# Kernel tuning notes

Hardware: AMD Instinct MI355X
Metric: run time of the kernel (lower is better)

Reference implementation:

```python
import jax, jax.numpy as jnp
import numpy as np
import math

H = 16          # num_heads
EPS = 1e-5      # LayerNorm eps (torch default)


def setup_inputs() -> dict:
    key = jax.random.key(0)
    ks = jax.random.split(key, 4)
    B, T, D = 2, 2048, 1024
    s = 1.0 / math.sqrt(D)
    return {
        "x": jax.random.normal(ks[0], (B, T, D), dtype=jnp.float32),
        "ln_g": jnp.ones((D,), jnp.float32),
        "ln_b": jnp.zeros((D,), jnp.float32),
        "Wq": jax.random.normal(ks[1], (D, D), jnp.float32) * s,
        "bq": jnp.zeros((D,), jnp.float32),
        "Wk": jax.random.normal(ks[2], (D, D), jnp.float32) * s,
        "bk": jnp.zeros((D,), jnp.float32),
        "Wv": jax.random.normal(ks[3], (D, D), jnp.float32) * s,
        "bv": jnp.zeros((D,), jnp.float32),
    }


def reference(x, ln_g, ln_b, Wq, bq, Wk, bk, Wv, bv):
    B, T, D = x.shape
    # LayerNorm (shared across the three projections, computed once)
    mu = jnp.mean(x, axis=-1, keepdims=True)
    var = jnp.mean(jnp.square(x - mu), axis=-1, keepdims=True)
    xn = (x - mu) * jax.lax.rsqrt(var + EPS) * ln_g + ln_b
    # Q/K/V projections -> [B, T, H, Dh]
    q = (xn @ Wq + bq).reshape(B, T, H, D // H)
    k = (xn @ Wk + bk).reshape(B, T, H, D // H)
    v = (xn @ Wv + bv).reshape(B, T, H, D // H)
    # QK^T scores [B, n, m, h], scaled by sqrt(head_dim)
    scale = 1.0 / math.sqrt(D // H)
    attn = jnp.einsum('bnhd,bmhd->bnmh', q, k) * scale
    # softmax over key axis (dim=2), dropout p=0 is identity
    w = jax.nn.softmax(attn, axis=2)
    # weighted sum of values, merge heads
    y = jnp.einsum('bnmh,bmhd->bnhd', w, v).reshape(B, T, D)
    return y
```

## Files before the change

### kernel.cpp

```cpp
#include <hip/hip_runtime.h>
#include <hip/hip_bf16.h>


typedef __attribute__((ext_vector_type(8)))  short short8;
typedef __attribute__((ext_vector_type(4)))  float f32x4;
typedef __attribute__((ext_vector_type(2)))  float f32x2;
typedef __attribute__((ext_vector_type(16))) float f32x16;
typedef __attribute__((ext_vector_type(2)))  unsigned int uint2v;

#define D_MODEL 1024
#define T_SEQ   2048
#define NHEAD   16
#define HDIM    64

#define LOG2E 1.4426950408889634f

__device__ __forceinline__ unsigned short f2bf(float x) {
    unsigned int u = __float_as_uint(x);
    u = (u + 0x7fffu + ((u >> 16) & 1u)) >> 16;
    return (unsigned short)u;
}

#if defined(__has_builtin)
#if __has_builtin(__builtin_amdgcn_permlane32_swap)
#define HAVE_PERMSWAP 1
#endif
#endif

__device__ __forceinline__ uint2v permswap(unsigned a, unsigned b) {
#ifdef HAVE_PERMSWAP
    return __builtin_amdgcn_permlane32_swap(a, b, false, false);
#else
    uint2v r;
    const unsigned as = (unsigned)__shfl_xor((int)a, 32, 64);
    const unsigned bs = (unsigned)__shfl_xor((int)b, 32, 64);
    const bool hi = (threadIdx.x & 32) != 0;
    r[0] = hi ? bs : a;
    r[1] = hi ? b  : as;
    return r;
#endif
}

__device__ __forceinline__ void group_barrier() {
    asm volatile("s_waitcnt lgkmcnt(0)" ::: "memory");
    __builtin_amdgcn_s_barrier();
    asm volatile("" ::: "memory");
}

__device__ __forceinline__ void w8(unsigned short* p, const uint4 v) {
    uint2 a; a.x = v.x; a.y = v.y;
    uint2 b; b.x = v.z; b.y = v.w;
    *(uint2*)p = a;
    *(uint2*)(p + 4) = b;
}

__device__ __forceinline__ short8 read8(const unsigned short* p) {
    union { unsigned u[4]; short8 s; } r;
    const uint2 a = *(const uint2*)p;
    const uint2 b = *(const uint2*)(p + 4);
    r.u[0] = a.x; r.u[1] = a.y; r.u[2] = b.x; r.u[3] = b.y;
    return r.s;
}

__global__ __launch_bounds__(256) void ln_wcast_kernel(
    const float* __restrict__ x, const float* __restrict__ gam,
    const float* __restrict__ bet, unsigned short* __restrict__ xn,
    const float* __restrict__ Wq, const float* __restrict__ Wk,
    const float* __restrict__ Wv, unsigned short* __restrict__ Wt)
{
    __shared__ float red[8];
    __shared__ float tile[32][33];
    const int bid = blockIdx.x;
    if (bid < 4096) {
        const int row = bid;
        const int t = threadIdx.x;
        const float4 v = ((const float4*)(x + (size_t)row * D_MODEL))[t];
        float s  = v.x + v.y + v.z + v.w;
        float s2 = v.x * v.x + v.y * v.y + v.z * v.z + v.w * v.w;
#pragma unroll
        for (int off = 32; off; off >>= 1) {
            s  += __shfl_down(s,  off, 64);
            s2 += __shfl_down(s2, off, 64);
        }
        const int lane = t & 63, wave = t >> 6;
        if (lane == 0) { red[wave] = s; red[4 + wave] = s2; }
        __syncthreads();
        s  = red[0] + red[1] + red[2] + red[3];
        s2 = red[4] + red[5] + red[6] + red[7];
        const float mu   = s * (1.f / D_MODEL);
        const float var  = s2 * (1.f / D_MODEL) - mu * mu;
        const float rstd = rsqrtf(var + 1e-5f);
        const float4 gv = ((const float4*)gam)[t];
        const float4 bv = ((const float4*)bet)[t];
        ushort4 o;
        o.x = f2bf((v.x - mu) * rstd * gv.x + bv.x);
        o.y = f2bf((v.y - mu) * rstd * gv.y + bv.y);
        o.z = f2bf((v.z - mu) * rstd * gv.z + bv.z);
        o.w = f2bf((v.w - mu) * rstd * gv.w + bv.w);
        ((ushort4*)(xn + (size_t)row * D_MODEL))[t] = o;
    } else {
        const int id = bid - 4096;
        const int z  = id >> 10;
        const int t2 = id & 1023;
        const int n0 = (t2 & 31) * 32, k0 = (t2 >> 5) * 32;
        const float* W = (z == 0) ? Wq : (z == 1) ? Wk : Wv;
        unsigned short* outw = Wt + (size_t)z * D_MODEL * D_MODEL;
        const int tx = threadIdx.x & 31, ty = threadIdx.x >> 5;
#pragma unroll
        for (int i = ty; i < 32; i += 8)
            tile[i][tx] = W[(size_t)(k0 + i) * D_MODEL + n0 + tx];
        __syncthreads();
#pragma unroll
        for (int i = ty; i < 32; i += 8)
            outw[(size_t)(n0 + i) * D_MODEL + k0 + tx] = f2bf(tile[tx][i]);
    }
}

__global__ __launch_bounds__(256) void qkv_gemm_kernel(
    const unsigned short* __restrict__ xn, const unsigned short* __restrict__ Wt,
    const float* __restrict__ bq, const float* __restrict__ bk, const float* __restrict__ bv,
    unsigned short* __restrict__ qo, unsigned short* __restrict__ ko, unsigned short* __restrict__ vt)
{
    const int which = blockIdx.x >> 3;
    const int xt = blockIdx.x & 7, yt = blockIdx.y;
    const bool vmode = (which == 2);
    const unsigned short* Aptr = vmode ? (Wt + (size_t)2 * D_MODEL * D_MODEL) : xn;
    const unsigned short* Bptr = vmode ? xn : (Wt + (size_t)which * D_MODEL * D_MODEL);
    const float* bias   = (which == 0) ? bq : (which == 1) ? bk : bv;
    const float scale   = (which == 0) ? (0.125f * LOG2E) : 1.0f;
    const int m0 = vmode ? xt * 128 : yt * 128;
    const int n0 = vmode ? yt * 128 : xt * 128;

    __shared__ unsigned short As[128][64];
    __shared__ unsigned short Bs[128][64];

    const int tid = threadIdx.x;
    const int lane = tid & 63, wave = tid >> 6;
    const int wr = wave >> 1, wc = wave & 1;
    const int g = lane >> 4, c = lane & 15;

    const int srow = lane >> 3;
    const int swzc = (((lane & 7) * 8) ^ ((srow & 7) * 8));
    const int rsw  = (c & 7) * 8;

    f32x4 acc[4][4] = {};

    for (int kt = 0; kt < D_MODEL; kt += 64) {
        __syncthreads();
#pragma unroll
        for (int i = 0; i < 4; ++i) {
            const int r = wave * 32 + i * 8;
            const unsigned short* ga = Aptr + (size_t)(m0 + r + srow) * D_MODEL + kt + swzc;
            __builtin_amdgcn_global_load_lds(
                (const __attribute__((address_space(1))) unsigned int*)ga,
                (__attribute__((address_space(3))) unsigned int*)(&As[r][0]), 16, 0, 0);
            const unsigned short* gb = Bptr + (size_t)(n0 + r + srow) * D_MODEL + kt + swzc;
            __builtin_amdgcn_global_load_lds(
                (const __attribute__((address_space(1))) unsigned int*)gb,
                (__attribute__((address_space(3))) unsigned int*)(&Bs[r][0]), 16, 0, 0);
        }
        __syncthreads();

        short8 af[4][2], bf[4][2];
#pragma unroll
        for (int i = 0; i < 4; ++i) {
            const int ra = wr * 64 + i * 16 + c;
            const int rb = wc * 64 + i * 16 + c;
#pragma unroll
            for (int kk = 0; kk < 2; ++kk) {
                af[i][kk] = *(const short8*)(&As[ra][(kk * 32 + g * 8) ^ rsw]);
                bf[i][kk] = *(const short8*)(&Bs[rb][(kk * 32 + g * 8) ^ rsw]);
            }
        }
#pragma unroll
        for (int kk = 0; kk < 2; ++kk)
#pragma unroll
            for (int i = 0; i < 4; ++i)
#pragma unroll
                for (int j = 0; j < 4; ++j)
                    acc[i][j] = __builtin_amdgcn_mfma_f32_16x16x32_bf16(
                        af[i][kk], bf[j][kk], acc[i][j], 0, 0, 0);
    }

    if (!vmode) {
        unsigned short* out = (which == 0) ? qo : ko;
#pragma unroll
        for (int j = 0; j < 4; ++j) {
            const int n = n0 + wc * 64 + j * 16 + c;
            const float bn = bias[n];
            const int h = n >> 6, dh = n & 63;
#pragma unroll
            for (int i = 0; i < 4; ++i) {
#pragma unroll
                for (int r = 0; r < 4; ++r) {
                    const int m = m0 + wr * 64 + i * 16 + g * 4 + r;
                    const int bb = m >> 11, t = m & 2047;
                    out[((size_t)(bb * NHEAD + h) * T_SEQ + t) * HDIM + dh] =
                        f2bf((acc[i][j][r] + bn) * scale);
                }
            }
        }
    } else {
#pragma unroll
        for (int i = 0; i < 4; ++i) {
#pragma unroll
            for (int r = 0; r < 4; ++r) {
                const int m = m0 + wr * 64 + i * 16 + g * 4 + r;
                const float bn = bias[m];
#pragma unroll
                for (int j = 0; j < 4; ++j) {
                    const int n = n0 + wc * 64 + j * 16 + c;
                    const int bb = n >> 11, t = n & 2047;
                    vt[(size_t)bb * (D_MODEL * T_SEQ) + (size_t)m * T_SEQ + t] =
                        f2bf(acc[i][j][r] + bn);
                }
            }
        }
    }
}

__global__ __launch_bounds__(512, 4) void attn_kernel(
    const unsigned short* __restrict__ qb, const unsigned short* __restrict__ kb,
    const unsigned short* __restrict__ vtb, float* __restrict__ out)
{
    const int id  = blockIdx.x;
    const int swz = (id & 7) * 64 + (id >> 3);
    const int qt  = swz & 15;
    const int bh  = swz >> 4;
    const int b = bh >> 4, head = bh & 15;
    const unsigned short* Q  = qb  + (size_t)bh * T_SEQ * HDIM;
    const unsigned short* Kp = kb  + (size_t)bh * T_SEQ * HDIM;
    const unsigned short* Vt = vtb + (size_t)b * (D_MODEL * T_SEQ)
                                   + (size_t)head * (HDIM * T_SEQ);

    __shared__ __align__(16) unsigned short smem[17664];

    const int tid = threadIdx.x, lane = tid & 63, wave = tid >> 6;
    const int grp = wave >> 2, w4 = wave & 3;
    const int q = lane & 31, h = lane >> 5;
    const int kvbase = grp * (T_SEQ / 2);

    const int gtid = tid & 255;
    const int sr = gtid >> 3;
    const int sc = (gtid & 7) * 8;

    unsigned short* gbase = &smem[grp * 8704];

    short8 qf[4];
    {
        const unsigned short* qp = Q + (size_t)(qt * 128 + w4 * 32 + q) * HDIM;
#pragma unroll
        for (int c = 0; c < 4; ++c)
            qf[c] = *(const short8*)(qp + c * 16 + h * 8);
    }

    float l_r = 0.f;
    f32x16 o[2] = {};

    const unsigned short* kp0 = Kp + (size_t)(kvbase + sr) * HDIM + sc;
    const unsigned short* vp0 = Vt + (size_t)sr * T_SEQ + kvbase + sc;
    uint4 kr0 = *(const uint4*)(kp0);
    uint4 kr1 = *(const uint4*)(kp0 + 32 * HDIM);
    uint4 vr0 = *(const uint4*)(vp0);
    uint4 vr1 = *(const uint4*)(vp0 + 32 * T_SEQ);
    w8(gbase + sr * 68 + sc, kr0);
    w8(gbase + (sr + 32) * 68 + sc, kr1);
    w8(gbase + 4352 + sr * 68 + sc, vr0);
    w8(gbase + 4352 + (sr + 32) * 68 + sc, vr1);
    kp0 += 64 * HDIM;
    vp0 += 64;

#pragma unroll 1
    for (int t = 0; t < 16; ++t) {
        const bool more = (t + 1 < 16);
        if (more) {
            kr0 = *(const uint4*)(kp0);
            kr1 = *(const uint4*)(kp0 + 32 * HDIM);
            vr0 = *(const uint4*)(vp0);
            vr1 = *(const uint4*)(vp0 + 32 * T_SEQ);
            kp0 += 64 * HDIM;
            vp0 += 64;
        }
        group_barrier();
        const unsigned short* kbuf = gbase;
        const unsigned short* vbuf = gbase + 4352;

        f32x16 s0 = {}, s1 = {};
        __builtin_amdgcn_s_setprio(1);
#pragma unroll
        for (int c = 0; c < 4; ++c) {
            const short8 kf0 = read8(kbuf + (size_t)q * 68 + c * 16 + h * 8);
            const short8 kf1 = read8(kbuf + (size_t)(32 + q) * 68 + c * 16 + h * 8);
            s0 = __builtin_amdgcn_mfma_f32_32x32x16_bf16(kf0, qf[c], s0, 0, 0, 0);
            s1 = __builtin_amdgcn_mfma_f32_32x32x16_bf16(kf1, qf[c], s1, 0, 0, 0);
        }
        __builtin_amdgcn_s_setprio(0);

#pragma unroll
        for (int r = 0; r < 16; ++r) { s0[r] = exp2f(s0[r]); }
#pragma unroll
        for (int r = 0; r < 16; ++r) { s1[r] = exp2f(s1[r]); }

        {
            f32x2 u[8];
#pragma unroll
            for (int r = 0; r < 8; ++r) {
                f32x2 a; a[0] = s0[2*r]; a[1] = s0[2*r+1];
                f32x2 bb; bb[0] = s1[2*r]; bb[1] = s1[2*r+1];
                u[r] = a + bb;
            }
            u[0] += u[1]; u[2] += u[3]; u[4] += u[5]; u[6] += u[7];
            u[0] += u[2]; u[4] += u[6];
            u[0] += u[4];
            float rs = u[0][0] + u[0][1];
            rs += __shfl_xor(rs, 32, 64);
            l_r += rs;
        }

        unsigned Wb0[8], Wb1[8];
#pragma unroll
        for (int u = 0; u < 4; ++u) {
            asm("v_cvt_pk_bf16_f32 %0, %1, %2" : "=v"(Wb0[u*2])   : "v"(s0[4*u]),   "v"(s0[4*u+1]));
            asm("v_cvt_pk_bf16_f32 %0, %1, %2" : "=v"(Wb0[u*2+1]) : "v"(s0[4*u+2]), "v"(s0[4*u+3]));
            asm("v_cvt_pk_bf16_f32 %0, %1, %2" : "=v"(Wb1[u*2])   : "v"(s1[4*u]),   "v"(s1[4*u+1]));
            asm("v_cvt_pk_bf16_f32 %0, %1, %2" : "=v"(Wb1[u*2+1]) : "v"(s1[4*u+2]), "v"(s1[4*u+3]));
        }

        short8 pf[4];
#pragma unroll
        for (int m = 0; m < 2; ++m) {
            {
                const uint2v r0 = permswap(Wb0[4*m],     Wb0[4*m + 2]);
                const uint2v r1 = permswap(Wb0[4*m + 1], Wb0[4*m + 3]);
                union { unsigned u[4]; short8 s; } pw;
                pw.u[0] = r0[0]; pw.u[1] = r1[0]; pw.u[2] = r0[1]; pw.u[3] = r1[1];
                pf[m] = pw.s;
            }
            {
                const uint2v r0 = permswap(Wb1[4*m],     Wb1[4*m + 2]);
                const uint2v r1 = permswap(Wb1[4*m + 1], Wb1[4*m + 3]);
                union { unsigned u[4]; short8 s; } pw;
                pw.u[0] = r0[0]; pw.u[1] = r1[0]; pw.u[2] = r0[1]; pw.u[3] = r1[1];
                pf[2 + m] = pw.s;
            }
        }

        __builtin_amdgcn_s_setprio(1);
#pragma unroll
        for (int dt = 0; dt < 2; ++dt) {
#pragma unroll
            for (int cp = 0; cp < 4; ++cp) {
                const short8 vf = read8(vbuf + (size_t)(dt * 32 + q) * 68 + cp * 16 + h * 8);
                o[dt] = __builtin_amdgcn_mfma_f32_32x32x16_bf16(vf, pf[cp], o[dt], 0, 0, 0);
            }
        }
        __builtin_amdgcn_s_setprio(0);

        group_barrier();
        if (more) {
            w8(gbase + sr * 68 + sc, kr0);
            w8(gbase + (sr + 32) * 68 + sc, kr1);
            w8(gbase + 4352 + sr * 68 + sc, vr0);
            w8(gbase + 4352 + (sr + 32) * 68 + sc, vr1);
        }
    }

    float* obuf  = (float*)(void*)smem;
    float* l_lds = ((float*)(void*)smem) + 128 * 68;

    const int qrl = w4 * 32 + q;
    if (grp == 0) {
#pragma unroll
        for (int dt = 0; dt < 2; ++dt)
#pragma unroll
            for (int u = 0; u < 4; ++u) {
                float* dst = obuf + (size_t)qrl * 68 + dt * 32 + 8 * u + 4 * h;
                float2 lo; lo.x = o[dt][4*u];     lo.y = o[dt][4*u + 1];
                float2 hi; hi.x = o[dt][4*u + 2]; hi.y = o[dt][4*u + 3];
                *(float2*)dst = lo;
                *(float2*)(dst + 2) = hi;
            }
        if (h == 0) l_lds[qrl] = l_r;
    }
    __syncthreads();
    if (grp == 1) {
        const float invl = 1.0f / (l_lds[qrl] + l_r);
#pragma unroll
        for (int dt = 0; dt < 2; ++dt)
#pragma unroll
            for (int u = 0; u < 4; ++u) {
                float* dst = obuf + (size_t)qrl * 68 + dt * 32 + 8 * u + 4 * h;
                float2 lo = *(const float2*)dst;
                float2 hi = *(const float2*)(dst + 2);
                lo.x = (lo.x + o[dt][4*u])     * invl;
                lo.y = (lo.y + o[dt][4*u + 1]) * invl;
                hi.x = (hi.x + o[dt][4*u + 2]) * invl;
                hi.y = (hi.y + o[dt][4*u + 3]) * invl;
                *(float2*)dst = lo;
                *(float2*)(dst + 2) = hi;
            }
    }
    __syncthreads();
#pragma unroll
    for (int it = 0; it < 4; ++it) {
        const int row = it * 32 + (tid >> 4);
        const int col = (tid & 15) * 4;
        const float4 v = *(const float4*)(&obuf[(size_t)row * 68 + col]);
        *(float4*)(&out[(size_t)(b * T_SEQ + qt * 128 + row) * D_MODEL + head * HDIM + col]) = v;
    }
}

extern "C" void kernel_launch(void* const* d_in, const int* in_sizes, int n_in,
                              void* d_out, int out_size, void* d_ws, size_t ws_size,
                              hipStream_t stream)
{
    const float* x   = (const float*)d_in[0];
    const float* lng = (const float*)d_in[1];
    const float* lnb = (const float*)d_in[2];
    const float* Wq  = (const float*)d_in[3];
    const float* bq  = (const float*)d_in[4];
    const float* Wk  = (const float*)d_in[5];
    const float* bk  = (const float*)d_in[6];
    const float* Wv  = (const float*)d_in[7];
    const float* bv  = (const float*)d_in[8];
    float* out = (float*)d_out;

    unsigned short* xn = (unsigned short*)d_ws;
    unsigned short* Wt = xn + (size_t)4096 * 1024;
    unsigned short* qh = Wt + (size_t)3 * 1024 * 1024;
    unsigned short* kh = qh + (size_t)4096 * 1024;
    unsigned short* vt = kh + (size_t)4096 * 1024;

    ln_wcast_kernel<<<7168, 256, 0, stream>>>(x, lng, lnb, xn, Wq, Wk, Wv, Wt);
    qkv_gemm_kernel<<<dim3(24, 32), 256, 0, stream>>>(xn, Wt, bq, bk, bv, qh, kh, vt);
    attn_kernel<<<512, 512, 0, stream>>>(qh, kh, vt, out);
}
```

Measured before the change: 110.0 us.

## Split attention KV range across four wave groups with 1024-thread blocks

Doubles the attention block from 512 to 1024 threads and splits the key/value sequence across four groups of four waves instead of two, so each group loops over 8 tiles instead of 16. Partial outputs and row sums from the four groups are combined through two LDS buffers, and normalisation moves into a final pass. This adds intra-block parallelism to shorten each block's serial KV loop. In exchange, LDS use per block roughly doubles and there is a larger cross-group reduction, which may limit how many blocks fit per CU.

```diff
diff --git a/kernel.cpp b/kernel.cpp
--- a/kernel.cpp
+++ b/kernel.cpp
@@ -219,7 +219,7 @@
     }
 }
 
-__global__ __launch_bounds__(512, 4) void attn_kernel(
+__global__ __launch_bounds__(1024, 8) void attn_kernel(
     const unsigned short* __restrict__ qb, const unsigned short* __restrict__ kb,
     const unsigned short* __restrict__ vtb, float* __restrict__ out)
 {
@@ -233,12 +233,12 @@
     const unsigned short* Vt = vtb + (size_t)b * (D_MODEL * T_SEQ)
                                    + (size_t)head * (HDIM * T_SEQ);
 
-    __shared__ __align__(16) unsigned short smem[17664];
+    __shared__ __align__(16) unsigned short smem[35840];
 
     const int tid = threadIdx.x, lane = tid & 63, wave = tid >> 6;
     const int grp = wave >> 2, w4 = wave & 3;
     const int q = lane & 31, h = lane >> 5;
-    const int kvbase = grp * (T_SEQ / 2);
+    const int kvbase = grp * (T_SEQ / 4);
 
     const int gtid = tid & 255;
     const int sr = gtid >> 3;
@@ -271,8 +271,8 @@
     vp0 += 64;
 
 #pragma unroll 1
-    for (int t = 0; t < 16; ++t) {
-        const bool more = (t + 1 < 16);
+    for (int t = 0; t < 8; ++t) {
+        const bool more = (t + 1 < 8);
         if (more) {
             kr0 = *(const uint4*)(kp0);
             kr1 = *(const uint4*)(kp0 + 32 * HDIM);
@@ -365,11 +365,15 @@
         }
     }
 
-    float* obuf  = (float*)(void*)smem;
-    float* l_lds = ((float*)(void*)smem) + 128 * 68;
+    float* obufA = (float*)(void*)smem;
+    float* obufB = (float*)(void*)(smem + 17408);
+    float* l_lds = (float*)(void*)(smem + 34816);
+    float* obuf  = (grp < 2) ? obufA : obufB;
 
     const int qrl = w4 * 32 + q;
-    if (grp == 0) {
+    __syncthreads();
+    if (h == 0) l_lds[grp * 128 + qrl] = l_r;
+    if ((grp & 1) == 0) {
 #pragma unroll
         for (int dt = 0; dt < 2; ++dt)
 #pragma unroll
@@ -380,11 +384,9 @@
                 *(float2*)dst = lo;
                 *(float2*)(dst + 2) = hi;
             }
-        if (h == 0) l_lds[qrl] = l_r;
     }
     __syncthreads();
-    if (grp == 1) {
-        const float invl = 1.0f / (l_lds[qrl] + l_r);
+    if ((grp & 1) == 1) {
 #pragma unroll
         for (int dt = 0; dt < 2; ++dt)
 #pragma unroll
@@ -392,21 +394,30 @@
                 float* dst = obuf + (size_t)qrl * 68 + dt * 32 + 8 * u + 4 * h;
                 float2 lo = *(const float2*)dst;
                 float2 hi = *(const float2*)(dst + 2);
-                lo.x = (lo.x + o[dt][4*u])     * invl;
-                lo.y = (lo.y + o[dt][4*u + 1]) * invl;
-                hi.x = (hi.x + o[dt][4*u + 2]) * invl;
-                hi.y = (hi.y + o[dt][4*u + 3]) * invl;
+                lo.x += o[dt][4*u];     lo.y += o[dt][4*u + 1];
+                hi.x += o[dt][4*u + 2]; hi.y += o[dt][4*u + 3];
                 *(float2*)dst = lo;
                 *(float2*)(dst + 2) = hi;
             }
     }
     __syncthreads();
-#pragma unroll
-    for (int it = 0; it < 4; ++it) {
-        const int row = it * 32 + (tid >> 4);
-        const int col = (tid & 15) * 4;
-        const float4 v = *(const float4*)(&obuf[(size_t)row * 68 + col]);
-        *(float4*)(&out[(size_t)(b * T_SEQ + qt * 128 + row) * D_MODEL + head * HDIM + col]) = v;
+    {
+        const int row = tid >> 3;
+        const int col = (tid & 7) * 8;
+        const float invl = 1.0f / (l_lds[row] + l_lds[128 + row] +
+                                   l_lds[256 + row] + l_lds[384 + row]);
+        const float4 a0 = *(const float4*)(obufA + (size_t)row * 68 + col);
+        const float4 a1 = *(const float4*)(obufA + (size_t)row * 68 + col + 4);
+        const float4 b0 = *(const float4*)(obufB + (size_t)row * 68 + col);
+        const float4 b1 = *(const float4*)(obufB + (size_t)row * 68 + col + 4);
+        float4 r0, r1;
+        r0.x = (a0.x + b0.x) * invl; r0.y = (a0.y + b0.y) * invl;
+        r0.z = (a0.z + b0.z) * invl; r0.w = (a0.w + b0.w) * invl;
+        r1.x = (a1.x + b1.x) * invl; r1.y = (a1.y + b1.y) * invl;
+        r1.z = (a1.z + b1.z) * invl; r1.w = (a1.w + b1.w) * invl;
+        float* op = &out[(size_t)(b * T_SEQ + qt * 128 + row) * D_MODEL + head * HDIM + col];
+        *(float4*)op = r0;
+        *(float4*)(op + 4) = r1;
     }
 }
 
@@ -433,5 +444,5 @@
 
     ln_wcast_kernel<<<7168, 256, 0, stream>>>(x, lng, lnb, xn, Wq, Wk, Wv, Wt);
     qkv_gemm_kernel<<<dim3(24, 32), 256, 0, stream>>>(xn, Wt, bq, bk, bv, qh, kh, vt);
-    attn_kernel<<<512, 512, 0, stream>>>(qh, kh, vt, out);
-}
+    attn_kernel<<<512, 1024, 0, stream>>>(qh, kh, vt, out);
+}
```

After: 394.9 us. 259% more time.
